# Performance work log

Hardware: AMD Instinct MI355X
Metric: run time of the kernel (lower is better)

The kernel has to match this reference:

```python
import jax, jax.numpy as jnp
import numpy as np

B, N, C_IN, L, C_OUT = 8, 50000, 32, 9, 64
M, NNZ = 12500, 37500


def setup_inputs() -> dict:
    key = jax.random.key(0)
    k = jax.random.split(key, 7)
    x = jax.random.normal(k[0], (B, N, C_IN), dtype=jnp.float32)
    weight = jax.random.normal(k[1], (L * C_IN, C_OUT), dtype=jnp.float32) * (1.0 / np.sqrt(L * C_IN))
    bias = jax.random.normal(k[2], (C_OUT,), dtype=jnp.float32) * 0.01
    values = jax.random.uniform(k[3], (NNZ,), dtype=jnp.float32)
    spiral_indices = jax.random.randint(k[4], (N, L), 0, N, dtype=jnp.int64)
    rows = jax.random.randint(k[5], (NNZ,), 0, M, dtype=jnp.int64)
    cols = jax.random.randint(k[6], (NNZ,), 0, N, dtype=jnp.int64)
    return {"x": x, "weight": weight, "bias": bias, "values": values,
            "spiral_indices": spiral_indices, "rows": rows, "cols": cols,
            "num_out_verts": M}


def reference(x, weight, bias, values, spiral_indices, rows, cols, num_out_verts):
    b, n, c = x.shape
    # SpiralConv: gather spiral neighborhoods, flatten, linear
    g = x[:, spiral_indices]                      # [B, N, L, C]
    g = g.reshape(b, n, -1)                       # [B, N, L*C]
    out = jnp.einsum('bnk,ko->bno', g, weight) + bias
    out = jax.nn.elu(out)                         # [B, N, C_OUT]
    # Pool: sparse down_transform (gather, scale, scatter_add)
    gathered = out[:, cols] * values[None, :, None]          # [B, NNZ, C_OUT]
    pooled = jnp.zeros((b, num_out_verts, out.shape[-1]), dtype=out.dtype)
    pooled = pooled.at[:, rows].add(gathered)                # [B, M, C_OUT]
    return pooled
```

## Files before the change

### kernel.cpp

```cpp
#include <hip/hip_runtime.h>

#define BATCH   8
#define NVERT   50000
#define CIN     32
#define LSP     9
#define COUT    64
#define MVERT   12500
#define NNZ     37500

#define NFRAG   2304
#define OUTDW   (BATCH * MVERT * COUT)

#define TILE_T  128
#define TPB     293

#define PRE_BLOCKS   6250
#define PACK_BLOCKS  9
#define ZERO_BLOCKS  6250
#define HISTA_BLOCKS 147

typedef __attribute__((ext_vector_type(8))) short  short8;
typedef __attribute__((ext_vector_type(4))) float  floatx4;

static __device__ __forceinline__ unsigned short f2bf(float f) {
    union { float f; unsigned int u; } c; c.f = f;
    unsigned int u = c.u;
    return (unsigned short)((u + 0x7fffu + ((u >> 16) & 1u)) >> 16);
}

__global__ __launch_bounds__(256)
void prep_kernel(const float* __restrict__ x, const float* __restrict__ w,
                 const int* __restrict__ rows,
                 unsigned short* __restrict__ x16, unsigned short* __restrict__ wp,
                 float* __restrict__ out, int* __restrict__ hist)
{
    const int blk = blockIdx.x;
    const int tid = threadIdx.x;
    if (blk < PRE_BLOCKS) {
        const size_t base = ((size_t)blk * 256 + tid) * 8;
        const float4* s = (const float4*)(x + base);
        float4 a = s[0], c = s[1];
        unsigned short t[8];
        t[0]=f2bf(a.x); t[1]=f2bf(a.y); t[2]=f2bf(a.z); t[3]=f2bf(a.w);
        t[4]=f2bf(c.x); t[5]=f2bf(c.y); t[6]=f2bf(c.z); t[7]=f2bf(c.w);
        *(uint4*)(x16 + base) = *(uint4*)t;
    } else if (blk < PRE_BLOCKS + PACK_BLOCKS) {
        const int f = (blk - PRE_BLOCKS) * 256 + tid;
        if (f < NFRAG) {
            int s = f >> 8, g = (f >> 6) & 3, lane = f & 63;
            int k0 = s * 32 + (lane >> 4) * 8, col = g * 16 + (lane & 15);
            unsigned short t[8];
            #pragma unroll
            for (int j = 0; j < 8; ++j)
                t[j] = f2bf(w[(size_t)(k0 + j) * COUT + col]);
            ((uint4*)wp)[f] = *(uint4*)t;
        }
    } else if (blk < PRE_BLOCKS + PACK_BLOCKS + ZERO_BLOCKS) {
        const size_t base = ((size_t)(blk - PRE_BLOCKS - PACK_BLOCKS) * 256 + tid) * 4;
        if (base < OUTDW) *(uint4*)(out + base) = (uint4){0, 0, 0, 0};
    } else {
        const int z = (blk - PRE_BLOCKS - PACK_BLOCKS - ZERO_BLOCKS) * 256 + tid;
        if (z < NNZ) atomicAdd(&hist[rows[z]], 1);
    }
}

__global__ __launch_bounds__(1024)
void scan_kernel(const int* __restrict__ hist, int* __restrict__ off2) {
    __shared__ int sh[1024];
    const int t = threadIdx.x;
    const int base = t * 13;
    int loc[13];
    int s = 0;
    #pragma unroll
    for (int j = 0; j < 13; ++j) {
        int i = base + j;
        int v = (i < MVERT) ? hist[i] : 0;
        loc[j] = s; s += v;
    }
    sh[t] = s;
    __syncthreads();
    for (int d = 1; d < 1024; d <<= 1) {
        int v = (t >= d) ? sh[t - d] : 0;
        __syncthreads();
        sh[t] += v;
        __syncthreads();
    }
    const int excl = sh[t] - s;
    #pragma unroll
    for (int j = 0; j < 13; ++j) {
        int i = base + j;
        if (i < MVERT) off2[i] = excl + loc[j];
    }
}

__global__ __launch_bounds__(256)
void scatter_kernel(const int* __restrict__ rows, const int* __restrict__ cols,
                    const float* __restrict__ vals, const int* __restrict__ spiral,
                    int* __restrict__ off2,
                    int* __restrict__ rows_s, float* __restrict__ vals_s,
                    unsigned short* __restrict__ tidx) {
    int z = blockIdx.x * 256 + threadIdx.x;
    if (z < NNZ) {
        int r = rows[z];
        int c = cols[z];
        int pos = atomicAdd(&off2[r], 1);
        rows_s[pos] = r;
        vals_s[pos] = vals[z];
        unsigned short t[16];
        #pragma unroll
        for (int s = 0; s < 9; ++s) t[s] = (unsigned short)spiral[c * LSP + s];
        #pragma unroll
        for (int s = 9; s < 16; ++s) t[s] = 0;
        uint4* dst = (uint4*)(tidx + (size_t)pos * 16);
        dst[0] = *(uint4*)t;
        dst[1] = *(uint4*)(t + 8);
    }
}

__global__ __launch_bounds__(256, 2)
void spiral_mfma8_kernel(const unsigned short* __restrict__ x16,
                         const uint4* __restrict__ wp4,
                         const float* __restrict__ bias,
                         const unsigned short* __restrict__ tidx,
                         const int* __restrict__ rows_s,
                         const float* __restrict__ vals_s,
                         float* __restrict__ out)
{
    __shared__ uint4 wl[NFRAG];

    const int bid  = blockIdx.x;
    const int b    = bid & 7;
    const int tile = bid >> 3;
    const int tid  = threadIdx.x;
    const int w    = tid >> 6;
    const int lane = tid & 63;
    const int quad = lane >> 4;
    const int m16  = lane & 15;
    const int z0w  = tile * TILE_T + 32 * w;

    #pragma unroll
    for (int i = 0; i < 9; ++i)
        wl[i * 256 + tid] = wp4[i * 256 + tid];

    const int   zc   = min(z0w + (lane & 31), NNZ - 1);
    const int   rowv = rows_s[zc];
    const float valv = vals_s[zc];
    const uint4 p0 = *(const uint4*)(tidx + (size_t)zc * 16);
    const unsigned int p1 = *(const unsigned int*)(tidx + (size_t)zc * 16 + 8);
    int idx[9];
    idx[0] = p0.x & 0xffff;  idx[1] = p0.x >> 16;
    idx[2] = p0.y & 0xffff;  idx[3] = p0.y >> 16;
    idx[4] = p0.z & 0xffff;  idx[5] = p0.z >> 16;
    idx[6] = p0.w & 0xffff;  idx[7] = p0.w >> 16;
    idx[8] = p1 & 0xffff;

    const unsigned short* xb = x16 + (size_t)b * NVERT * CIN;

    short8 A[2][9];
    #pragma unroll
    for (int s = 0; s < 9; ++s) {
        #pragma unroll
        for (int mt = 0; mt < 2; ++mt) {
            int tix = __shfl(idx[s], mt * 16 + m16);
            A[mt][s] = *(const short8*)(xb + (size_t)tix * CIN + quad * 8);
        }
    }

    floatx4 acc[2][4];
    #pragma unroll
    for (int mt = 0; mt < 2; ++mt)
        #pragma unroll
        for (int g = 0; g < 4; ++g) acc[mt][g] = (floatx4){0.f, 0.f, 0.f, 0.f};

    __syncthreads();

    const unsigned short* wls = (const unsigned short*)wl;
    #pragma unroll
    for (int s = 0; s < 9; ++s) {
        short8 bf[4];
        #pragma unroll
        for (int g = 0; g < 4; ++g)
            bf[g] = *(const short8*)(wls + (size_t)((s * 4 + g) * 64 + lane) * 8);
        #pragma unroll
        for (int mt = 0; mt < 2; ++mt)
            #pragma unroll
            for (int g = 0; g < 4; ++g)
                acc[mt][g] = __builtin_amdgcn_mfma_f32_16x16x32_bf16(A[mt][s], bf[g], acc[mt][g], 0, 0, 0);
    }

    float bs[4];
    #pragma unroll
    for (int g = 0; g < 4; ++g) bs[g] = bias[g * 16 + m16];
    float* outb = out + (size_t)b * MVERT * COUT;

    #pragma unroll
    for (int mt = 0; mt < 2; ++mt) {
        int   rr[4]; float vv[4]; bool val[4];
        #pragma unroll
        for (int r = 0; r < 4; ++r) {
            const int tsk = mt * 16 + quad * 4 + r;
            rr[r]  = __shfl(rowv, tsk);
            vv[r]  = __shfl(valv, tsk);
            val[r] = (z0w + tsk) < NNZ;
        }
        bool emit[4];
        #pragma unroll
        for (int r = 0; r < 4; ++r)
            emit[r] = (r == 3) || (!val[r + 1 > 3 ? 3 : r + 1]) || (rr[r + 1 > 3 ? 3 : r + 1] != rr[r]);
        #pragma unroll
        for (int g = 0; g < 4; ++g) {
            const int ch = g * 16 + m16;
            float s = 0.0f;
            #pragma unroll
            for (int r = 0; r < 4; ++r) {
                if (val[r]) {
                    float y = acc[mt][g][r] + bs[g];
                    y = (y > 0.0f) ? y : (__expf(y) - 1.0f);
                    s += y * vv[r];
                    if (emit[r]) {
                        atomicAdd(outb + (size_t)rr[r] * COUT + ch, s);
                        s = 0.0f;
                    }
                }
            }
        }
    }
}

extern "C" void kernel_launch(void* const* d_in, const int* in_sizes, int n_in,
                              void* d_out, int out_size, void* d_ws, size_t ws_size,
                              hipStream_t stream) {
    const float* x      = (const float*)d_in[0];
    const float* w      = (const float*)d_in[1];
    const float* bias   = (const float*)d_in[2];
    const float* vals   = (const float*)d_in[3];
    const int*   spiral = (const int*)d_in[4];
    const int*   rows   = (const int*)d_in[5];
    const int*   cols   = (const int*)d_in[6];
    float* out = (float*)d_out;

    char* base = (char*)d_ws;
    unsigned short* wp     = (unsigned short*)(base);
    unsigned short* x16    = (unsigned short*)(base + 36864);
    int*            hist   = (int*)(base + 25636864);
    int*            off2   = (int*)(base + 25686864);
    int*            rows_s = (int*)(base + 25736864);
    float*          vals_s = (float*)(base + 26036896);
    unsigned short* tidx   = (unsigned short*)(base + 26186912);

    hipMemsetAsync(hist, 0, MVERT * sizeof(int), stream);

    const int prep_grid = PRE_BLOCKS + PACK_BLOCKS + ZERO_BLOCKS + HISTA_BLOCKS;
    prep_kernel<<<prep_grid, 256, 0, stream>>>(x, w, rows, x16, wp, out, hist);
    scan_kernel<<<1, 1024, 0, stream>>>(hist, off2);
    scatter_kernel<<<147, 256, 0, stream>>>(rows, cols, vals, spiral, off2,
                                            rows_s, vals_s, tidx);
    spiral_mfma8_kernel<<<BATCH * TPB, 256, 0, stream>>>(x16, (const uint4*)wp,
                                                         bias, tidx,
                                                         rows_s, vals_s, out);
}
```

Before: 172.9 us.

## Drop row-sorting pipeline, build spiral index table in prep, read weights from global

Removes the histogram, scan and scatter kernels (and the memset) that sorted nonzeros by output row. The spiral index table is now built inside the prep kernel in original nonzero order. The main MFMA kernel reads rows and values directly and loads weight fragments from global memory instead of staging them in LDS, raising the occupancy hint to 3. This cuts three launches and serial dependencies, at the cost of less coalesced scatter atomics without row sorting and weight reads that go through cache rather than LDS.

```diff
diff --git a/kernel.cpp b/kernel.cpp
--- a/kernel.cpp
+++ b/kernel.cpp
@@ -17,7 +17,7 @@
 #define PRE_BLOCKS   6250
 #define PACK_BLOCKS  9
 #define ZERO_BLOCKS  6250
-#define HISTA_BLOCKS 147
+#define TIDX_BLOCKS  147
 
 typedef __attribute__((ext_vector_type(8))) short  short8;
 typedef __attribute__((ext_vector_type(4))) float  floatx4;
@@ -30,9 +30,9 @@
 
 __global__ __launch_bounds__(256)
 void prep_kernel(const float* __restrict__ x, const float* __restrict__ w,
-                 const int* __restrict__ rows,
+                 const int* __restrict__ cols, const int* __restrict__ spiral,
                  unsigned short* __restrict__ x16, unsigned short* __restrict__ wp,
-                 float* __restrict__ out, int* __restrict__ hist)
+                 float* __restrict__ out, unsigned short* __restrict__ tidx)
 {
     const int blk = blockIdx.x;
     const int tid = threadIdx.x;
@@ -60,74 +60,29 @@
         if (base < OUTDW) *(uint4*)(out + base) = (uint4){0, 0, 0, 0};
     } else {
         const int z = (blk - PRE_BLOCKS - PACK_BLOCKS - ZERO_BLOCKS) * 256 + tid;
-        if (z < NNZ) atomicAdd(&hist[rows[z]], 1);
-    }
-}
-
-__global__ __launch_bounds__(1024)
-void scan_kernel(const int* __restrict__ hist, int* __restrict__ off2) {
-    __shared__ int sh[1024];
-    const int t = threadIdx.x;
-    const int base = t * 13;
-    int loc[13];
-    int s = 0;
-    #pragma unroll
-    for (int j = 0; j < 13; ++j) {
-        int i = base + j;
-        int v = (i < MVERT) ? hist[i] : 0;
-        loc[j] = s; s += v;
-    }
-    sh[t] = s;
-    __syncthreads();
-    for (int d = 1; d < 1024; d <<= 1) {
-        int v = (t >= d) ? sh[t - d] : 0;
-        __syncthreads();
-        sh[t] += v;
-        __syncthreads();
-    }
-    const int excl = sh[t] - s;
-    #pragma unroll
-    for (int j = 0; j < 13; ++j) {
-        int i = base + j;
-        if (i < MVERT) off2[i] = excl + loc[j];
-    }
-}
-
-__global__ __launch_bounds__(256)
-void scatter_kernel(const int* __restrict__ rows, const int* __restrict__ cols,
-                    const float* __restrict__ vals, const int* __restrict__ spiral,
-                    int* __restrict__ off2,
-                    int* __restrict__ rows_s, float* __restrict__ vals_s,
-                    unsigned short* __restrict__ tidx) {
-    int z = blockIdx.x * 256 + threadIdx.x;
-    if (z < NNZ) {
-        int r = rows[z];
-        int c = cols[z];
-        int pos = atomicAdd(&off2[r], 1);
-        rows_s[pos] = r;
-        vals_s[pos] = vals[z];
-        unsigned short t[16];
-        #pragma unroll
-        for (int s = 0; s < 9; ++s) t[s] = (unsigned short)spiral[c * LSP + s];
-        #pragma unroll
-        for (int s = 9; s < 16; ++s) t[s] = 0;
-        uint4* dst = (uint4*)(tidx + (size_t)pos * 16);
-        dst[0] = *(uint4*)t;
-        dst[1] = *(uint4*)(t + 8);
-    }
-}
-
-__global__ __launch_bounds__(256, 2)
-void spiral_mfma8_kernel(const unsigned short* __restrict__ x16,
-                         const uint4* __restrict__ wp4,
-                         const float* __restrict__ bias,
-                         const unsigned short* __restrict__ tidx,
-                         const int* __restrict__ rows_s,
-                         const float* __restrict__ vals_s,
-                         float* __restrict__ out)
+        if (z < NNZ) {
+            const int c = cols[z];
+            unsigned short t[16];
+            #pragma unroll
+            for (int s = 0; s < 9; ++s) t[s] = (unsigned short)spiral[c * LSP + s];
+            #pragma unroll
+            for (int s = 9; s < 16; ++s) t[s] = 0;
+            uint4* dst = (uint4*)(tidx + (size_t)z * 16);
+            dst[0] = *(uint4*)t;
+            dst[1] = *(uint4*)(t + 8);
+        }
+    }
+}
+
+__global__ __launch_bounds__(256, 3)
+void spiral_mfma12_kernel(const unsigned short* __restrict__ x16,
+                          const unsigned short* __restrict__ wp,
+                          const float* __restrict__ bias,
+                          const unsigned short* __restrict__ tidx,
+                          const int* __restrict__ rows,
+                          const float* __restrict__ vals,
+                          float* __restrict__ out)
 {
-    __shared__ uint4 wl[NFRAG];
-
     const int bid  = blockIdx.x;
     const int b    = bid & 7;
     const int tile = bid >> 3;
@@ -138,13 +93,9 @@
     const int m16  = lane & 15;
     const int z0w  = tile * TILE_T + 32 * w;
 
-    #pragma unroll
-    for (int i = 0; i < 9; ++i)
-        wl[i * 256 + tid] = wp4[i * 256 + tid];
-
     const int   zc   = min(z0w + (lane & 31), NNZ - 1);
-    const int   rowv = rows_s[zc];
-    const float valv = vals_s[zc];
+    const int   rowv = rows[zc];
+    const float valv = vals[zc];
     const uint4 p0 = *(const uint4*)(tidx + (size_t)zc * 16);
     const unsigned int p1 = *(const unsigned int*)(tidx + (size_t)zc * 16 + 8);
     int idx[9];
@@ -172,15 +123,12 @@
         #pragma unroll
         for (int g = 0; g < 4; ++g) acc[mt][g] = (floatx4){0.f, 0.f, 0.f, 0.f};
 
-    __syncthreads();
-
-    const unsigned short* wls = (const unsigned short*)wl;
     #pragma unroll
     for (int s = 0; s < 9; ++s) {
         short8 bf[4];
         #pragma unroll
         for (int g = 0; g < 4; ++g)
-            bf[g] = *(const short8*)(wls + (size_t)((s * 4 + g) * 64 + lane) * 8);
+            bf[g] = *(const short8*)(wp + (size_t)((s * 4 + g) * 64 + lane) * 8);
         #pragma unroll
         for (int mt = 0; mt < 2; ++mt)
             #pragma unroll
@@ -242,20 +190,11 @@
     char* base = (char*)d_ws;
     unsigned short* wp     = (unsigned short*)(base);
     unsigned short* x16    = (unsigned short*)(base + 36864);
-    int*            hist   = (int*)(base + 25636864);
-    int*            off2   = (int*)(base + 25686864);
-    int*            rows_s = (int*)(base + 25736864);
-    float*          vals_s = (float*)(base + 26036896);
     unsigned short* tidx   = (unsigned short*)(base + 26186912);
 
-    hipMemsetAsync(hist, 0, MVERT * sizeof(int), stream);
-
-    const int prep_grid = PRE_BLOCKS + PACK_BLOCKS + ZERO_BLOCKS + HISTA_BLOCKS;
-    prep_kernel<<<prep_grid, 256, 0, stream>>>(x, w, rows, x16, wp, out, hist);
-    scan_kernel<<<1, 1024, 0, stream>>>(hist, off2);
-    scatter_kernel<<<147, 256, 0, stream>>>(rows, cols, vals, spiral, off2,
-                                            rows_s, vals_s, tidx);
-    spiral_mfma8_kernel<<<BATCH * TPB, 256, 0, stream>>>(x16, (const uint4*)wp,
-                                                         bias, tidx,
-                                                         rows_s, vals_s, out);
-}
+    const int prep_grid = PRE_BLOCKS + PACK_BLOCKS + ZERO_BLOCKS + TIDX_BLOCKS;
+    prep_kernel<<<prep_grid, 256, 0, stream>>>(x, w, cols, spiral,
+                                               x16, wp, out, tidx);
+    spiral_mfma12_kernel<<<BATCH * TPB, 256, 0, stream>>>(x16, wp, bias, tidx,
+                                                          rows, vals, out);
+}
```

Measured after the change: 182.4 us. 1.05x slower.
